# Kernel optimization log

Measured on AMD Instinct MI355X. Metric: run time of the kernel, lower is better.

Reference implementation:

```python
import jax, jax.numpy as jnp
import numpy as np

N_ATOMS = 100000
N_BONDS = 200000
MAX_NB = 6
ATOM_FDIM = 133
BOND_FDIM = 147
HIDDEN = 300
DEPTH = 3
N_MOLS = 4000


def setup_inputs() -> dict:
    key = jax.random.key(0)
    ks = jax.random.split(key, 10)
    f_atoms = jax.random.normal(ks[0], (N_ATOMS, ATOM_FDIM), dtype=jnp.float32)
    f_bonds = jax.random.normal(ks[1], (N_BONDS, BOND_FDIM), dtype=jnp.float32)
    a2b = jax.random.randint(ks[2], (N_ATOMS, MAX_NB), 0, N_BONDS, dtype=jnp.int32)
    b2a = jax.random.randint(ks[3], (N_BONDS,), 0, N_ATOMS, dtype=jnp.int32)
    b2revb = jax.random.randint(ks[4], (N_BONDS,), 0, N_BONDS, dtype=jnp.int32)
    mol_ids = jnp.sort(jax.random.randint(ks[5], (N_ATOMS,), 0, N_MOLS, dtype=jnp.int32))
    # learned params (W_i, W_h have bias=False; W_o has bias)
    sc = 0.02
    W_i = jax.random.normal(ks[6], (BOND_FDIM, HIDDEN), dtype=jnp.float32) * sc
    W_h = jax.random.normal(ks[7], (HIDDEN, HIDDEN), dtype=jnp.float32) * sc
    W_o = jax.random.normal(ks[8], (ATOM_FDIM + HIDDEN, HIDDEN), dtype=jnp.float32) * sc
    b_o = jax.random.normal(ks[9], (HIDDEN,), dtype=jnp.float32) * sc
    return {"f_atoms": f_atoms, "f_bonds": f_bonds, "a2b": a2b, "b2a": b2a,
            "b2revb": b2revb, "mol_ids": mol_ids, "W_i": W_i, "W_h": W_h,
            "W_o": W_o, "b_o": b_o}


def reference(f_atoms, f_bonds, a2b, b2a, b2revb, mol_ids, W_i, W_h, W_o, b_o):
    # input = W_i(f_bonds); message = relu(input)
    inp = f_bonds @ W_i                              # [n_bonds, H]
    message = jax.nn.relu(inp)
    for _ in range(DEPTH - 1):
        # gather incoming-bond messages per atom and sum over neighbors
        a_message = message[a2b].sum(axis=1)         # [n_atoms, H]
        # directed-bond update: m_b = sum_in(src atom) - reverse message
        message = a_message[b2a] - message[b2revb]   # [n_bonds, H]
        message = jax.nn.relu(inp + message @ W_h)   # dropout p=0 -> identity
    a_message = message[a2b].sum(axis=1)             # [n_atoms, H]
    a_input = jnp.concatenate([f_atoms, a_message], axis=1)
    atom_hiddens = jax.nn.relu(a_input @ W_o + b_o)  # [n_atoms, H]
    # per-molecule mean aggregation (a_scope loop -> segment ops)
    sums = jax.ops.segment_sum(atom_hiddens, mol_ids, num_segments=N_MOLS)
    counts = jax.ops.segment_sum(jnp.ones((atom_hiddens.shape[0], 1), atom_hiddens.dtype),
                                 mol_ids, num_segments=N_MOLS)
    # empty molecules -> cached zero vector
    return jnp.where(counts > 0, sums / jnp.maximum(counts, 1.0), 0.0)
```

## Files before the change

### kernel.cpp

```cpp
#include <hip/hip_runtime.h>

typedef unsigned short bfraw;
typedef __attribute__((ext_vector_type(8))) short short8v;
typedef __attribute__((ext_vector_type(8))) unsigned short ushort8v;
typedef __attribute__((ext_vector_type(4))) float f32x4;

static __device__ __forceinline__ float bf2f(unsigned short u) {
    union { unsigned int i; float f; } c; c.i = ((unsigned int)u) << 16; return c.f;
}
static __device__ __forceinline__ unsigned short f2bf(float f) {
    union { float f; unsigned int i; } c; c.f = f;
    unsigned int r = c.i + 0x7fffu + ((c.i >> 16) & 1u);
    return (unsigned short)(r >> 16);
}
static __device__ __forceinline__ unsigned short brelu(unsigned short u) {
    return (u & 0x8000u) ? (unsigned short)0 : u;
}
static __device__ __forceinline__ f32x4 mfma16(short8v a, short8v b, f32x4 c) {
    return __builtin_amdgcn_mfma_f32_16x16x32_bf16(a, b, c, 0, 0, 0);
}

__global__ __launch_bounds__(64) void k_pack(const float* __restrict__ W, int Krows, int row_off,
                                             bfraw* __restrict__ out) {
    const int b = blockIdx.x;
    const int ks = b / 20, ct = b - ks * 20;
    const int l = threadIdx.x;
    const int n = ct * 16 + (l & 15);
    const int kb = ks * 32 + (l >> 4) * 8;
    short8v pk;
#pragma unroll
    for (int j = 0; j < 8; ++j) {
        int k = kb + j;
        float v = (k < Krows && n < 300) ? W[(row_off + k) * 300 + n] : 0.f;
        pk[j] = (short)f2bf(v);
    }
    *(short8v*)&out[(b * 64 + l) * 8] = pk;
}


__global__ __launch_bounds__(512, 4) void k_in(const float* __restrict__ fb,
                                               const bfraw* __restrict__ Wp,
                                               bfraw* __restrict__ inp) {
    __shared__ short A[64 * 40 * 8];
    const int row0 = blockIdx.x * 64;
    const int tid = threadIdx.x;
    if (tid < 128) {
        int r = tid >> 1, c = 18 + (tid & 1);
        short8v z = {0, 0, 0, 0, 0, 0, 0, 0};
        *(short8v*)&A[(r * 40 + (c ^ (r & 7))) * 8] = z;
    }
    __syncthreads();
    const float4* fb4 = (const float4*)(fb + (long long)row0 * 147);
#pragma unroll 1
    for (int s = 0; s < 5; ++s) {
        int idx = tid + s * 512;
        if (idx < 2352) {
            float4 v = fb4[idx];
            const float* ve = (const float*)&v;
            int k0 = idx * 4;
#pragma unroll
            for (int e = 0; e < 4; ++e) {
                int k = k0 + e;
                int r = k / 147;
                int c = k - r * 147;
                A[(r * 40 + ((c >> 3) ^ (r & 7))) * 8 + (c & 7)] = (short)f2bf(ve[e]);
            }
        }
    }
    __syncthreads();
    const int w = tid >> 6, l = tid & 63;
    const int wr = w >> 2, wc = w & 3;
    const int lr = l & 15, lk = l >> 4, sw = l & 7;
    f32x4 acc[2][5];
#pragma unroll
    for (int ri = 0; ri < 2; ++ri)
#pragma unroll
        for (int i = 0; i < 5; ++i) acc[ri][i] = (f32x4){0.f, 0.f, 0.f, 0.f};
    const short8v* Ald = (const short8v*)A;
#pragma unroll
    for (int ks = 0; ks < 5; ++ks) {
        short8v bfr[2], wv[5];
#pragma unroll
        for (int ri = 0; ri < 2; ++ri)
            bfr[ri] = Ald[((wr * 2 + ri) * 16 + lr) * 40 + ((ks * 4 + lk) ^ sw)];
#pragma unroll
        for (int i = 0; i < 5; ++i)
            wv[i] = *(const short8v*)&Wp[((ks * 20 + wc * 5 + i) * 64 + l) * 8];
#pragma unroll
        for (int ri = 0; ri < 2; ++ri)
#pragma unroll
            for (int i = 0; i < 5; ++i)
                acc[ri][i] = mfma16(wv[i], bfr[ri], acc[ri][i]);
    }
    __syncthreads();
#pragma unroll
    for (int ri = 0; ri < 2; ++ri)
#pragma unroll
        for (int i = 0; i < 5; ++i) {
            const int r = (wr * 2 + ri) * 16 + lr;
            const int c16 = (wc * 5 + i) * 2 + (lk >> 1);
            ushort4 t;
            t.x = f2bf(acc[ri][i][0]); t.y = f2bf(acc[ri][i][1]);
            t.z = f2bf(acc[ri][i][2]); t.w = f2bf(acc[ri][i][3]);
            *(ushort4*)&A[(r * 40 + (c16 ^ (r & 7))) * 8 + (lk & 1) * 4] = t;
        }
    __syncthreads();
    for (int idx = tid; idx < 64 * 38; idx += 512) {
        int r = idx / 38, c = idx - r * 38;
        short8v t = *(const short8v*)&A[(r * 40 + (c ^ (r & 7))) * 8];
        *(short8v*)&inp[(long long)(row0 + r) * 304 + c * 8] = t;
    }
}

__global__ __launch_bounds__(512, 4) void k_bond(const bfraw* __restrict__ msg,
                                                 const bfraw* __restrict__ inp,
                                                 const int* __restrict__ a2b,
                                                 const int* __restrict__ b2a,
                                                 const int* __restrict__ b2revb,
                                                 const bfraw* __restrict__ Wp,
                                                 bfraw* __restrict__ out) {
    __shared__ short A[64 * 40 * 8];
    const int row0 = blockIdx.x * 64;
    const int tid = threadIdx.x;
    if (tid < 128) {
        int r = tid >> 1, c = 38 + (tid & 1);
        short8v z = {0, 0, 0, 0, 0, 0, 0, 0};
        *(short8v*)&A[(r * 40 + (c ^ (r & 7))) * 8] = z;
    }
    ushort8v pf[5];
#pragma unroll
    for (int s = 0; s < 5; ++s) {
        int idx = tid + s * 512;
        if (idx < 64 * 38) {
            int r = idx / 38, c = idx - r * 38;
            pf[s] = *(const ushort8v*)&inp[(long long)(row0 + r) * 304 + c * 8];
        }
    }
#pragma unroll 1
    for (int s = 0; s < 5; ++s) {
        int idx = tid + s * 512;
        if (idx < 64 * 38) {
            int r = idx / 38, c = idx - r * 38;
            const int b = row0 + r;
            const int a = b2a[b];
            const int rv = b2revb[b];
            const int* nb = a2b + a * 6;
            float s8[8];
            const ushort8v vm = *(const ushort8v*)&msg[(long long)rv * 304 + c * 8];
#pragma unroll
            for (int e = 0; e < 8; ++e) s8[e] = -bf2f(brelu(vm[e]));
#pragma unroll
            for (int j = 0; j < 6; ++j) {
                const ushort8v v = *(const ushort8v*)&msg[(long long)nb[j] * 304 + c * 8];
#pragma unroll
                for (int e = 0; e < 8; ++e) s8[e] += bf2f(brelu(v[e]));
            }
            short8v pk;
#pragma unroll
            for (int e = 0; e < 8; ++e) pk[e] = (short)f2bf(s8[e]);
            *(short8v*)&A[(r * 40 + (c ^ (r & 7))) * 8] = pk;
        }
    }
    __syncthreads();
    const int w = tid >> 6, l = tid & 63;
    const int wr = w >> 2, wc = w & 3;
    const int lr = l & 15, lk = l >> 4, sw = l & 7;
    f32x4 acc[2][5];
#pragma unroll
    for (int ri = 0; ri < 2; ++ri)
#pragma unroll
        for (int i = 0; i < 5; ++i) acc[ri][i] = (f32x4){0.f, 0.f, 0.f, 0.f};
    const short8v* Ald = (const short8v*)A;
#pragma unroll
    for (int ks = 0; ks < 10; ++ks) {
        short8v bfr[2], wv[5];
#pragma unroll
        for (int ri = 0; ri < 2; ++ri)
            bfr[ri] = Ald[((wr * 2 + ri) * 16 + lr) * 40 + ((ks * 4 + lk) ^ sw)];
#pragma unroll
        for (int i = 0; i < 5; ++i)
            wv[i] = *(const short8v*)&Wp[((ks * 20 + wc * 5 + i) * 64 + l) * 8];
#pragma unroll
        for (int ri = 0; ri < 2; ++ri)
#pragma unroll
            for (int i = 0; i < 5; ++i)
                acc[ri][i] = mfma16(wv[i], bfr[ri], acc[ri][i]);
    }
    __syncthreads();
#pragma unroll
    for (int ri = 0; ri < 2; ++ri)
#pragma unroll
        for (int i = 0; i < 5; ++i) {
            const int r = (wr * 2 + ri) * 16 + lr;
            const int c16 = (wc * 5 + i) * 2 + (lk >> 1);
            ushort4 t;
            t.x = f2bf(acc[ri][i][0]); t.y = f2bf(acc[ri][i][1]);
            t.z = f2bf(acc[ri][i][2]); t.w = f2bf(acc[ri][i][3]);
            *(ushort4*)&A[(r * 40 + (c16 ^ (r & 7))) * 8 + (lk & 1) * 4] = t;
        }
    __syncthreads();
#pragma unroll
    for (int s = 0; s < 5; ++s) {
        int idx = tid + s * 512;
        if (idx < 64 * 38) {
            int r = idx / 38, c = idx - r * 38;
            short8v t = *(const short8v*)&A[(r * 40 + (c ^ (r & 7))) * 8];
            short8v m;
#pragma unroll
            for (int j = 0; j < 8; ++j)
                m[j] = (short)f2bf(bf2f(pf[s][j]) + bf2f((unsigned short)t[j]));
            *(short8v*)&out[(long long)(row0 + r) * 304 + c * 8] = m;
        }
    }
}

__global__ __launch_bounds__(512, 4) void k_out(const float* __restrict__ fa,
                                                const bfraw* __restrict__ msg,
                                                const int* __restrict__ a2b,
                                                const bfraw* __restrict__ WfP,
                                                const bfraw* __restrict__ WaP,
                                                const float* __restrict__ bo,
                                                bfraw* __restrict__ hid) {
    __shared__ short A[64 * 40 * 8];
    const int row0 = blockIdx.x * 64;
    const int tid = threadIdx.x;
#pragma unroll
    for (int it = 0; it < 5; ++it) {
        int idx = tid + it * 512;
        int r = idx / 40, c = idx - r * 40;
        const int row = row0 + r;
        short8v pk;
        if (c < 38 && row < 100000) {
            const int* nb = a2b + row * 6;
            float s[8];
#pragma unroll
            for (int e = 0; e < 8; ++e) s[e] = 0.f;
#pragma unroll
            for (int j = 0; j < 6; ++j) {
                const ushort8v v = *(const ushort8v*)&msg[(long long)nb[j] * 304 + c * 8];
#pragma unroll
                for (int e = 0; e < 8; ++e) s[e] += bf2f(brelu(v[e]));
            }
#pragma unroll
            for (int e = 0; e < 8; ++e) pk[e] = (short)f2bf(s[e]);
        } else {
#pragma unroll
            for (int j = 0; j < 8; ++j) pk[j] = 0;
        }
        *(short8v*)&A[(r * 40 + (c ^ (r & 7))) * 8] = pk;
    }
    __syncthreads();
    const int w = tid >> 6, l = tid & 63;
    const int wr = w >> 2, wc = w & 3;
    const int lr = l & 15, lk = l >> 4, sw = l & 7;
    f32x4 acc[2][5];
#pragma unroll
    for (int ri = 0; ri < 2; ++ri)
#pragma unroll
        for (int i = 0; i < 5; ++i) acc[ri][i] = (f32x4){0.f, 0.f, 0.f, 0.f};
    const short8v* Ald = (const short8v*)A;
#pragma unroll
    for (int ks = 0; ks < 10; ++ks) {
        short8v bfr[2], wv[5];
#pragma unroll
        for (int ri = 0; ri < 2; ++ri)
            bfr[ri] = Ald[((wr * 2 + ri) * 16 + lr) * 40 + ((ks * 4 + lk) ^ sw)];
#pragma unroll
        for (int i = 0; i < 5; ++i)
            wv[i] = *(const short8v*)&WaP[((ks * 20 + wc * 5 + i) * 64 + l) * 8];
#pragma unroll
        for (int ri = 0; ri < 2; ++ri)
#pragma unroll
            for (int i = 0; i < 5; ++i)
                acc[ri][i] = mfma16(wv[i], bfr[ri], acc[ri][i]);
    }
    __syncthreads();
    for (int idx = tid; idx < 64 * 20; idx += 512) {
        int r = idx / 20, c = idx - r * 20;
        const int row = row0 + r;
        const int kbase = c * 8;
        short8v pk;
        if (row < 100000) {
            const float* src = fa + (long long)row * 133 + kbase;
#pragma unroll
            for (int j = 0; j < 8; ++j) {
                float v = (kbase + j < 133) ? src[j] : 0.f;
                pk[j] = (short)f2bf(v);
            }
        } else {
#pragma unroll
            for (int j = 0; j < 8; ++j) pk[j] = 0;
        }
        *(short8v*)&A[(r * 40 + (c ^ (r & 7))) * 8] = pk;
    }
    __syncthreads();
#pragma unroll
    for (int ks = 0; ks < 5; ++ks) {
        short8v bfr[2], wv[5];
#pragma unroll
        for (int ri = 0; ri < 2; ++ri)
            bfr[ri] = Ald[((wr * 2 + ri) * 16 + lr) * 40 + ((ks * 4 + lk) ^ sw)];
#pragma unroll
        for (int i = 0; i < 5; ++i)
            wv[i] = *(const short8v*)&WfP[((ks * 20 + wc * 5 + i) * 64 + l) * 8];
#pragma unroll
        for (int ri = 0; ri < 2; ++ri)
#pragma unroll
            for (int i = 0; i < 5; ++i)
                acc[ri][i] = mfma16(wv[i], bfr[ri], acc[ri][i]);
    }
    __syncthreads();
#pragma unroll
    for (int ri = 0; ri < 2; ++ri)
#pragma unroll
        for (int i = 0; i < 5; ++i) {
            const int r = (wr * 2 + ri) * 16 + lr;
            const int c16 = (wc * 5 + i) * 2 + (lk >> 1);
            ushort4 t;
            t.x = f2bf(acc[ri][i][0]); t.y = f2bf(acc[ri][i][1]);
            t.z = f2bf(acc[ri][i][2]); t.w = f2bf(acc[ri][i][3]);
            *(ushort4*)&A[(r * 40 + (c16 ^ (r & 7))) * 8 + (lk & 1) * 4] = t;
        }
    __syncthreads();
    for (int idx = tid; idx < 64 * 38; idx += 512) {
        int r = idx / 38, c = idx - r * 38;
        const int row = row0 + r;
        if (row >= 100000) continue;
        short8v t = *(const short8v*)&A[(r * 40 + (c ^ (r & 7))) * 8];
        float4 b0 = *(const float4*)&bo[c * 8];
        float4 b1 = (c < 37) ? *(const float4*)&bo[c * 8 + 4]
                             : make_float4(0.f, 0.f, 0.f, 0.f);
        float bias[8] = {b0.x, b0.y, b0.z, b0.w, b1.x, b1.y, b1.z, b1.w};
        short8v m;
#pragma unroll
        for (int j = 0; j < 8; ++j)
            m[j] = (short)f2bf(fmaxf(bf2f((unsigned short)t[j]) + bias[j], 0.f));
        *(short8v*)&hid[(long long)row * 304 + c * 8] = m;
    }
}

__global__ __launch_bounds__(320) void k_mean(const bfraw* __restrict__ hid,
                                              const int* __restrict__ mol,
                                              float* __restrict__ out) {
    __shared__ float red[8][304];
    const int m = blockIdx.x;
    const int natoms = 100000;
    int lo = 0, hi = natoms;
    while (lo < hi) { int mid = (lo + hi) >> 1; if (mol[mid] < m) lo = mid + 1; else hi = mid; }
    const int start = lo;
    lo = start; hi = natoms;
    while (lo < hi) { int mid = (lo + hi) >> 1; if (mol[mid] <= m) lo = mid + 1; else hi = mid; }
    const int end = lo;
    const int tid = threadIdx.x;
    const int p = tid / 38, c = tid - p * 38;
    if (tid < 304) {
        float s[8];
#pragma unroll
        for (int e = 0; e < 8; ++e) s[e] = 0.f;
        for (int a = start + p; a < end; a += 8) {
            const ushort8v v = *(const ushort8v*)&hid[(long long)a * 304 + c * 8];
#pragma unroll
            for (int e = 0; e < 8; ++e) s[e] += bf2f(v[e]);
        }
#pragma unroll
        for (int e = 0; e < 8; ++e) red[p][c * 8 + e] = s[e];
    }
    __syncthreads();
    if (tid < 300) {
        float t = 0.f;
#pragma unroll
        for (int p2 = 0; p2 < 8; ++p2) t += red[p2][tid];
        const int n = end - start;
        out[m * 300 + tid] = (n > 0) ? (t / (float)n) : 0.f;
    }
}

extern "C" void kernel_launch(void* const* d_in, const int* in_sizes, int n_in,
                              void* d_out, int out_size, void* d_ws, size_t ws_size,
                              hipStream_t stream) {
    const float* f_atoms = (const float*)d_in[0];
    const float* f_bonds = (const float*)d_in[1];
    const int* a2b      = (const int*)d_in[2];
    const int* b2a      = (const int*)d_in[3];
    const int* b2revb   = (const int*)d_in[4];
    const int* mol_ids  = (const int*)d_in[5];
    const float* W_i    = (const float*)d_in[6];
    const float* W_h    = (const float*)d_in[7];
    const float* W_o    = (const float*)d_in[8];
    const float* b_o    = (const float*)d_in[9];
    float* out = (float*)d_out;

    char* wsb = (char*)d_ws;
    bfraw* inp  = (bfraw*)(wsb);
    bfraw* M1   = (bfraw*)(wsb + 121600000ll);
    bfraw* M2   = (bfraw*)(wsb + 243200000ll);
    bfraw* WiP   = (bfraw*)(wsb + 425600000ll);
    bfraw* WhP   = (bfraw*)(wsb + 425702400ll);
    bfraw* WoFaP = (bfraw*)(wsb + 425907200ll);
    bfraw* WoAmP = (bfraw*)(wsb + 426009600ll);

    k_pack<<<100, 64, 0, stream>>>(W_i, 147, 0, WiP);
    k_pack<<<200, 64, 0, stream>>>(W_h, 300, 0, WhP);
    k_pack<<<100, 64, 0, stream>>>(W_o, 133, 0, WoFaP);
    k_pack<<<200, 64, 0, stream>>>(W_o, 300, 133, WoAmP);

    const int nb_blocks = 200000 / 64;
    const int na_blocks = (100000 + 63) / 64;

    k_in<<<nb_blocks, 512, 0, stream>>>(f_bonds, WiP, inp);
    k_bond<<<nb_blocks, 512, 0, stream>>>(inp, inp, a2b, b2a, b2revb, WhP, M1);
    k_bond<<<nb_blocks, 512, 0, stream>>>(M1, inp, a2b, b2a, b2revb, WhP, M2);

    bfraw* hid = M1;
    k_out<<<na_blocks, 512, 0, stream>>>(f_atoms, M2, a2b, WoFaP, WoAmP, b_o, hid);
    k_mean<<<4000, 320, 0, stream>>>(hid, mol_ids, out);
}
```

Before: 688.2 us.

## Precompute per-atom neighbor message sums in separate gather kernel

Measured after the change: 603.3 us. -12.3%, faster.

```diff
diff --git a/kernel.cpp b/kernel.cpp
--- a/kernel.cpp
+++ b/kernel.cpp
@@ -112,9 +112,37 @@
     }
 }
 
-__global__ __launch_bounds__(512, 4) void k_bond(const bfraw* __restrict__ msg,
+__global__ __launch_bounds__(256) void k_gather(const bfraw* __restrict__ msg,
+                                                const int* __restrict__ a2b,
+                                                bfraw* __restrict__ amsg) {
+    int gid = blockIdx.x * 256 + threadIdx.x;
+    if (gid >= 100000 * 19) return;
+    int a = gid / 19, c = gid - a * 19;
+    const int* nb = a2b + a * 6;
+    float s0[8], s1[8];
+#pragma unroll
+    for (int e = 0; e < 8; ++e) { s0[e] = 0.f; s1[e] = 0.f; }
+#pragma unroll
+    for (int j = 0; j < 6; ++j) {
+        const long long base = (long long)nb[j] * 304;
+        const ushort8v v0 = *(const ushort8v*)&msg[base + c * 8];
+        const ushort8v v1 = *(const ushort8v*)&msg[base + (c + 19) * 8];
+#pragma unroll
+        for (int e = 0; e < 8; ++e) {
+            s0[e] += bf2f(brelu(v0[e]));
+            s1[e] += bf2f(brelu(v1[e]));
+        }
+    }
+    short8v o0, o1;
+#pragma unroll
+    for (int e = 0; e < 8; ++e) { o0[e] = (short)f2bf(s0[e]); o1[e] = (short)f2bf(s1[e]); }
+    *(short8v*)&amsg[(long long)a * 304 + c * 8] = o0;
+    *(short8v*)&amsg[(long long)a * 304 + (c + 19) * 8] = o1;
+}
+
+__global__ __launch_bounds__(512, 4) void k_bond(const bfraw* __restrict__ amsg,
+                                                 const bfraw* __restrict__ msg,
                                                  const bfraw* __restrict__ inp,
-                                                 const int* __restrict__ a2b,
                                                  const int* __restrict__ b2a,
                                                  const int* __restrict__ b2revb,
                                                  const bfraw* __restrict__ Wp,
@@ -127,38 +155,35 @@
         short8v z = {0, 0, 0, 0, 0, 0, 0, 0};
         *(short8v*)&A[(r * 40 + (c ^ (r & 7))) * 8] = z;
     }
-    ushort8v pf[5];
-#pragma unroll
-    for (int s = 0; s < 5; ++s) {
-        int idx = tid + s * 512;
-        if (idx < 64 * 38) {
-            int r = idx / 38, c = idx - r * 38;
-            pf[s] = *(const ushort8v*)&inp[(long long)(row0 + r) * 304 + c * 8];
-        }
-    }
-#pragma unroll 1
-    for (int s = 0; s < 5; ++s) {
-        int idx = tid + s * 512;
-        if (idx < 64 * 38) {
-            int r = idx / 38, c = idx - r * 38;
-            const int b = row0 + r;
-            const int a = b2a[b];
-            const int rv = b2revb[b];
-            const int* nb = a2b + a * 6;
-            float s8[8];
-            const ushort8v vm = *(const ushort8v*)&msg[(long long)rv * 304 + c * 8];
-#pragma unroll
-            for (int e = 0; e < 8; ++e) s8[e] = -bf2f(brelu(vm[e]));
-#pragma unroll
-            for (int j = 0; j < 6; ++j) {
-                const ushort8v v = *(const ushort8v*)&msg[(long long)nb[j] * 304 + c * 8];
-#pragma unroll
-                for (int e = 0; e < 8; ++e) s8[e] += bf2f(brelu(v[e]));
-            }
+    int rr[5], cc[5], ia[5], irv[5];
+#pragma unroll
+    for (int s = 0; s < 5; ++s) {
+        int idx = tid + s * 512;
+        if (s < 4 || idx < 2432) {
+            rr[s] = idx / 38; cc[s] = idx - rr[s] * 38;
+            const int b = row0 + rr[s];
+            ia[s] = b2a[b];
+            irv[s] = b2revb[b];
+        }
+    }
+    ushort8v va[5], vm[5];
+#pragma unroll
+    for (int s = 0; s < 5; ++s) {
+        int idx = tid + s * 512;
+        if (s < 4 || idx < 2432) {
+            va[s] = *(const ushort8v*)&amsg[(long long)ia[s] * 304 + cc[s] * 8];
+            vm[s] = *(const ushort8v*)&msg[(long long)irv[s] * 304 + cc[s] * 8];
+        }
+    }
+#pragma unroll
+    for (int s = 0; s < 5; ++s) {
+        int idx = tid + s * 512;
+        if (s < 4 || idx < 2432) {
             short8v pk;
 #pragma unroll
-            for (int e = 0; e < 8; ++e) pk[e] = (short)f2bf(s8[e]);
-            *(short8v*)&A[(r * 40 + (c ^ (r & 7))) * 8] = pk;
+            for (int j = 0; j < 8; ++j)
+                pk[j] = (short)f2bf(bf2f(va[s][j]) - bf2f(brelu(vm[s][j])));
+            *(short8v*)&A[(rr[s] * 40 + (cc[s] ^ (rr[s] & 7))) * 8] = pk;
         }
     }
     __syncthreads();
@@ -199,16 +224,25 @@
             *(ushort4*)&A[(r * 40 + (c16 ^ (r & 7))) * 8 + (lk & 1) * 4] = t;
         }
     __syncthreads();
-#pragma unroll
-    for (int s = 0; s < 5; ++s) {
-        int idx = tid + s * 512;
-        if (idx < 64 * 38) {
+    ushort8v ip[5];
+#pragma unroll
+    for (int s = 0; s < 5; ++s) {
+        int idx = tid + s * 512;
+        if (s < 4 || idx < 2432) {
+            int r = idx / 38, c = idx - r * 38;
+            ip[s] = *(const ushort8v*)&inp[(long long)(row0 + r) * 304 + c * 8];
+        }
+    }
+#pragma unroll
+    for (int s = 0; s < 5; ++s) {
+        int idx = tid + s * 512;
+        if (s < 4 || idx < 2432) {
             int r = idx / 38, c = idx - r * 38;
             short8v t = *(const short8v*)&A[(r * 40 + (c ^ (r & 7))) * 8];
             short8v m;
 #pragma unroll
             for (int j = 0; j < 8; ++j)
-                m[j] = (short)f2bf(bf2f(pf[s][j]) + bf2f((unsigned short)t[j]));
+                m[j] = (short)f2bf(bf2f(ip[s][j]) + bf2f((unsigned short)t[j]));
             *(short8v*)&out[(long long)(row0 + r) * 304 + c * 8] = m;
         }
     }
@@ -224,6 +258,7 @@
     __shared__ short A[64 * 40 * 8];
     const int row0 = blockIdx.x * 64;
     const int tid = threadIdx.x;
+    const int nvalid = (row0 + 64 <= 100000) ? 64 : (100000 - row0);
 #pragma unroll
     for (int it = 0; it < 5; ++it) {
         int idx = tid + it * 512;
@@ -275,23 +310,31 @@
                 acc[ri][i] = mfma16(wv[i], bfr[ri], acc[ri][i]);
     }
     __syncthreads();
-    for (int idx = tid; idx < 64 * 20; idx += 512) {
-        int r = idx / 20, c = idx - r * 20;
-        const int row = row0 + r;
-        const int kbase = c * 8;
-        short8v pk;
-        if (row < 100000) {
-            const float* src = fa + (long long)row * 133 + kbase;
-#pragma unroll
-            for (int j = 0; j < 8; ++j) {
-                float v = (kbase + j < 133) ? src[j] : 0.f;
-                pk[j] = (short)f2bf(v);
+    if (tid < 256) {
+        int r = tid >> 2, c = 16 + (tid & 3);
+        short8v z = {0, 0, 0, 0, 0, 0, 0, 0};
+        *(short8v*)&A[(r * 40 + (c ^ (r & 7))) * 8] = z;
+    }
+    __syncthreads();
+    {
+        const float4* fa4 = (const float4*)(fa + (long long)row0 * 133);
+        const int limit4 = (nvalid * 133) >> 2;
+#pragma unroll 1
+        for (int s = 0; s < 5; ++s) {
+            int idx = tid + s * 512;
+            if (idx < limit4) {
+                float4 v = fa4[idx];
+                const float* ve = (const float*)&v;
+                int k0 = idx * 4;
+#pragma unroll
+                for (int e = 0; e < 4; ++e) {
+                    int k = k0 + e;
+                    int r = k / 133;
+                    int c = k - r * 133;
+                    A[(r * 40 + ((c >> 3) ^ (r & 7))) * 8 + (c & 7)] = (short)f2bf(ve[e]);
+                }
             }
-        } else {
-#pragma unroll
-            for (int j = 0; j < 8; ++j) pk[j] = 0;
-        }
-        *(short8v*)&A[(r * 40 + (c ^ (r & 7))) * 8] = pk;
+        }
     }
     __syncthreads();
 #pragma unroll
@@ -394,6 +437,7 @@
     bfraw* inp  = (bfraw*)(wsb);
     bfraw* M1   = (bfraw*)(wsb + 121600000ll);
     bfraw* M2   = (bfraw*)(wsb + 243200000ll);
+    bfraw* amsg = (bfraw*)(wsb + 364800000ll);
     bfraw* WiP   = (bfraw*)(wsb + 425600000ll);
     bfraw* WhP   = (bfraw*)(wsb + 425702400ll);
     bfraw* WoFaP = (bfraw*)(wsb + 425907200ll);
@@ -406,10 +450,14 @@
 
     const int nb_blocks = 200000 / 64;
     const int na_blocks = (100000 + 63) / 64;
+    const int gather_blocks = (100000 * 19 + 255) / 256;
 
     k_in<<<nb_blocks, 512, 0, stream>>>(f_bonds, WiP, inp);
-    k_bond<<<nb_blocks, 512, 0, stream>>>(inp, inp, a2b, b2a, b2revb, WhP, M1);
-    k_bond<<<nb_blocks, 512, 0, stream>>>(M1, inp, a2b, b2a, b2revb, WhP, M2);
+
+    k_gather<<<gather_blocks, 256, 0, stream>>>(inp, a2b, amsg);
+    k_bond<<<nb_blocks, 512, 0, stream>>>(amsg, inp, inp, b2a, b2revb, WhP, M1);
+    k_gather<<<gather_blocks, 256, 0, stream>>>(M1, a2b, amsg);
+    k_bond<<<nb_blocks, 512, 0, stream>>>(amsg, M1, inp, b2a, b2revb, WhP, M2);
 
     bfraw* hid = M1;
     k_out<<<na_blocks, 512, 0, stream>>>(f_atoms, M2, a2b, WoFaP, WoAmP, b_o, hid);
```
